# Optimization experiments

Measured on AMD Instinct MI355X. Metric: run time of the kernel, lower is better.

Reference implementation:

```python
import jax, jax.numpy as jnp
import numpy as np

B, Z, A = 1024, 512, 8          # batch_size, z_dim, action_dim
AH, ZH = 64, 512                # action_hidden_dim, z_hidden_dim
N_NEG = 100                     # n_neg_actions
TEMP = 0.1                      # temperature
TOP_K = (1, 3, 10)


def forward_model(z, a, Wa, ba, W1, b1, W2, b2):
    # MLP forward model with skip connection (z_delta=True):
    # embed action, concat with z, 2-layer MLP predicting a delta.
    h_a = jax.nn.relu(a @ Wa + ba)                                   # [..., AH]
    h = jax.nn.relu(jnp.concatenate([jnp.broadcast_to(z, a.shape[:-1] + (Z,)), h_a], axis=-1) @ W1 + b1)  # [..., ZH]
    delta = h @ W2 + b2                                              # [..., Z]
    return z + delta


def setup_inputs() -> dict:
    key = jax.random.key(0)
    ks = jax.random.split(key, 8)
    def w(k, shape, fan_in):
        return jax.random.normal(k, shape, jnp.float32) / np.float32(np.sqrt(fan_in))
    z = jax.random.normal(ks[0], (B, Z), jnp.float32)
    z_next = jax.random.normal(ks[1], (B, Z), jnp.float32)
    z_next_hat = jax.random.normal(ks[2], (B, Z), jnp.float32)
    actions = jax.random.normal(ks[3], (B, A), jnp.float32)
    Wa = w(ks[4], (A, AH), A)
    ba = jnp.zeros((AH,), jnp.float32)
    W1 = w(ks[5], (Z + AH, ZH), Z + AH)
    b1 = jnp.zeros((ZH,), jnp.float32)
    W2 = w(ks[6], (ZH, Z), ZH)
    b2 = jnp.zeros((Z,), jnp.float32)
    return {"z": z, "z_next": z_next, "z_next_hat": z_next_hat, "actions": actions,
            "Wa": Wa, "ba": ba, "W1": W1, "b1": b1, "W2": W2, "b2": b2}


def reference(z, z_next, z_next_hat, actions, Wa, ba, W1, b1, W2, b2):
    # ControlCPC.compute_loss with dot_product_similarity, vectorized:
    # the Python loop over n_neg_actions rolled-action forward-model calls
    # becomes one batched [n-1, B, ...] forward-model evaluation.
    batch = z.shape[0]
    n = min(N_NEG, batch)
    sim = z_next @ z_next_hat.T                                      # [B, B] positives on diagonal
    shifts = jnp.arange(1, n)
    neg_actions = jax.vmap(lambda i: jnp.roll(actions, -i, axis=0))(shifts)  # [n-1, B, A]
    z_hat_neg = forward_model(z[None], neg_actions, Wa, ba, W1, b1, W2, b2)  # [n-1, B, Z]
    neg_sim = jnp.einsum('nbz,bz->bn', z_hat_neg, z_next)            # diag of similarity per shift
    sim_mat = jnp.concatenate([sim, neg_sim], axis=1)                # [B, B+n-1]
    # INCE loss, positives on diagonal
    logp = jax.nn.log_softmax(sim_mat / jnp.float32(TEMP), axis=1)
    loss = -jnp.mean(jnp.diagonal(logp))                             # diagonal takes first B entries
    labels = jnp.arange(batch)[:, None]
    accs = []
    for k in TOP_K:
        _, preds = jax.lax.top_k(sim_mat, k)                         # [B, k]
        accs.append(jnp.mean((preds == labels).astype(jnp.float32)) * k)
    return (loss, accs[0], accs[1], accs[2])
```

## Files before the change

kernel.cpp:

```cpp
#include <hip/hip_runtime.h>
#include <math.h>

#define B_SZ 1024
#define Z_DIM 512
#define A_DIM 8
#define AH 64
#define ZH 512
#define NNEG 99
#define INV_T 10.0f
#define RNP 104

typedef __attribute__((ext_vector_type(8))) short short8;
typedef __attribute__((ext_vector_type(4))) short short4b;
typedef __attribute__((ext_vector_type(4))) float f32x4;

__device__ __forceinline__ short bf16rn(float x) {
    unsigned u = __float_as_uint(x);
    u += 0x7fffu + ((u >> 16) & 1u);
    return (short)(u >> 16);
}
__device__ __forceinline__ void cvt8rn(float4 x0, float4 x1, short8& h) {
    h[0] = bf16rn(x0.x); h[1] = bf16rn(x0.y); h[2] = bf16rn(x0.z); h[3] = bf16rn(x0.w);
    h[4] = bf16rn(x1.x); h[5] = bf16rn(x1.y); h[6] = bf16rn(x1.z); h[7] = bf16rn(x1.w);
}

__device__ __forceinline__ int sw(int m, int kb) { return m * 8 + (kb ^ (m & 7)); }

#define VMWAIT(N) asm volatile("s_waitcnt vmcnt(" #N ")" ::: "memory")
__device__ __forceinline__ void raw_barrier() {
    asm volatile("" ::: "memory");
    __builtin_amdgcn_s_barrier();
    asm volatile("" ::: "memory");
}
typedef const __attribute__((address_space(1))) void* gas_ptr;
typedef __attribute__((address_space(3))) void* las_ptr;
__device__ __forceinline__ void gld_lds16(const void* gsrc, void* ldst) {
    __builtin_amdgcn_global_load_lds((gas_ptr)gsrc, (las_ptr)ldst, 16, 0, 0);
}

__global__ __launch_bounds__(256) void cvt_kernel(
    const float* __restrict__ z, const float* __restrict__ z_next,
    const float* __restrict__ z_next_hat, const float* __restrict__ W1,
    const float* __restrict__ W2, const float* __restrict__ actions,
    const float* __restrict__ Wa, const float* __restrict__ ba,
    short* __restrict__ zb, short* __restrict__ znb, short* __restrict__ znhb,
    short* __restrict__ w1t, short* __restrict__ w2b, short* __restrict__ hab)
{
    const int id = blockIdx.x, tid = threadIdx.x;
    if (id < 896) {
        const float* src; short* dst; int local;
        if (id < 256)      { src = z;          dst = zb;   local = id; }
        else if (id < 512) { src = z_next;     dst = znb;  local = id - 256; }
        else if (id < 768) { src = z_next_hat; dst = znhb; local = id - 512; }
        else               { src = W2;         dst = w2b;  local = id - 768; }
        int i8 = local * 2048 + tid * 8;
        float4 x0 = *(const float4*)&src[i8];
        float4 x1 = *(const float4*)&src[i8 + 4];
        short8 h; cvt8rn(x0, x1, h);
        *(short8*)&dst[i8] = h;
    } else if (id < 968) {
        __shared__ float L[64][68];
        int local = id - 896, kt = local >> 3, nt = local & 7;
#pragma unroll
        for (int i = 0; i < 4; ++i) {
            int f = tid + i * 256;
            int r = f >> 4, c4 = (f & 15) << 2;
            *(float4*)&L[r][c4] = *(const float4*)&W1[(kt * 64 + r) * 512 + nt * 64 + c4];
        }
        __syncthreads();
#pragma unroll
        for (int i = 0; i < 4; ++i) {
            int f = tid + i * 256;
            int r = f >> 4, c4 = (f & 15) << 2;
            short4b o = {bf16rn(L[c4][r]), bf16rn(L[c4 + 1][r]),
                         bf16rn(L[c4 + 2][r]), bf16rn(L[c4 + 3][r])};
            *(short4b*)&w1t[(nt * 64 + r) * 576 + kt * 64 + c4] = o;
        }
    } else {
        __shared__ float sWa[A_DIM * 64];
        __shared__ float sba[64];
        int j0 = (id - 968) * 64;
        for (int i = tid; i < A_DIM * 64; i += 256) sWa[i] = Wa[i];
        if (tid < 64) sba[tid] = ba[tid];
        __syncthreads();
        int r = tid >> 2, c0 = (tid & 3) * 16;
        float4 a0 = *(const float4*)&actions[(j0 + r) * A_DIM + 0];
        float4 a1 = *(const float4*)&actions[(j0 + r) * A_DIM + 4];
        float av[8] = {a0.x, a0.y, a0.z, a0.w, a1.x, a1.y, a1.z, a1.w};
        float o[16];
#pragma unroll
        for (int c = 0; c < 16; ++c) o[c] = sba[c0 + c];
#pragma unroll
        for (int k = 0; k < A_DIM; ++k)
#pragma unroll
            for (int c = 0; c < 16; ++c) o[c] += av[k] * sWa[k * 64 + c0 + c];
#pragma unroll
        for (int c = 0; c < 16; c += 4) {
            short4b h = {bf16rn(fmaxf(o[c], 0.f)),     bf16rn(fmaxf(o[c + 1], 0.f)),
                         bf16rn(fmaxf(o[c + 2], 0.f)), bf16rn(fmaxf(o[c + 3], 0.f))};
            *(short4b*)&hab[(j0 + r) * 64 + c0 + c] = h;
        }
    }
}

__global__ __launch_bounds__(256, 2) void mm_kernel(
    const short* __restrict__ zb, const short* __restrict__ znb,
    const short* __restrict__ znhb, const short* __restrict__ w1t,
    const short* __restrict__ w2b, const short* __restrict__ hab,
    const float* __restrict__ b1,
    float* __restrict__ sim, float* __restrict__ u, float* __restrict__ v,
    float* __restrict__ g)
{
    __shared__ __align__(16) short Ah[128 * 64], Bh[128 * 64];

    const int id = blockIdx.x;
    const int tid = threadIdx.x;

    const short* A; const short* B; const float* bias = nullptr;
    float* C; int N, K, lda, ldb, bm0, bn0;
    if (id < 64) {
        bm0 = (id >> 3) * 128; bn0 = (id & 7) * 128;
        A = znb; lda = 512; B = znhb; ldb = 512; C = sim; N = 1024; K = 512;
    } else if (id < 96) {
        int t = id - 64; bm0 = (t >> 2) * 128; bn0 = (t & 3) * 128;
        A = zb; lda = 512; B = w1t; ldb = 576; C = u; N = 512; K = 512; bias = b1;
    } else if (id < 128) {
        int t = id - 96; bm0 = (t >> 2) * 128; bn0 = (t & 3) * 128;
        A = znb; lda = 512; B = w2b; ldb = 512; C = v; N = 512; K = 512;
    } else {
        int t = id - 128; bm0 = (t >> 2) * 128; bn0 = (t & 3) * 128;
        A = hab; lda = 64; B = w1t + 512; ldb = 576; C = g; N = 512; K = 64;
    }

    const int lane = tid & 63, wv = tid >> 6;
    const int lm = lane & 15, lq = lane >> 4;
    const int wr = (wv >> 1) * 64, wc = (wv & 1) * 64;
    short8* A8 = (short8*)Ah; short8* B8 = (short8*)Bh;
    f32x4 acc[4][4] = {};

    for (int k0 = 0; k0 < K; k0 += 64) {
#pragma unroll
        for (int q = 0; q < 4; ++q) {
            int f = q * 256 + tid;
            int row = f >> 3;
            int ug = (f & 7) ^ (row & 7);
            gld_lds16(&A[(bm0 + row) * lda + k0 + ug * 8],
                      &Ah[(q * 256 + wv * 64) * 8]);
            gld_lds16(&B[(bn0 + row) * ldb + k0 + ug * 8],
                      &Bh[(q * 256 + wv * 64) * 8]);
        }
        VMWAIT(0);
        raw_barrier();
#pragma unroll
        for (int kk = 0; kk < 64; kk += 32) {
            int kbi = (kk >> 3) + lq;
            short8 ah[4], bh[4];
#pragma unroll
            for (int i = 0; i < 4; ++i) ah[i] = A8[sw(wr + i * 16 + lm, kbi)];
#pragma unroll
            for (int j = 0; j < 4; ++j) bh[j] = B8[sw(wc + j * 16 + lm, kbi)];
#pragma unroll
            for (int i = 0; i < 4; ++i)
#pragma unroll
                for (int j = 0; j < 4; ++j)
                    acc[i][j] = __builtin_amdgcn_mfma_f32_16x16x32_bf16(ah[i], bh[j], acc[i][j], 0, 0, 0);
        }
        raw_barrier();
    }
#pragma unroll
    for (int i = 0; i < 4; ++i)
#pragma unroll
        for (int j = 0; j < 4; ++j) {
            int n = bn0 + wc + j * 16 + lm;
            float bb = bias ? bias[n] : 0.0f;
#pragma unroll
            for (int r = 0; r < 4; ++r) {
                int m = bm0 + wr + i * 16 + lq * 4 + r;
                C[m * N + n] = acc[i][j][r] + bb;
            }
        }
}

__global__ __launch_bounds__(64, 4) void neg_kernel(
    const float* __restrict__ u, const float* __restrict__ v,
    const float* __restrict__ g, float* __restrict__ rnall)
{
    const int b = blockIdx.x, t = blockIdx.y;
    const int lane = threadIdx.x;
    const int s0 = 1 + t * 8;

    float4 ga[8], gb[8];
#pragma unroll
    for (int c = 0; c < 8; ++c) {
        int j = (b + s0 + c) & (B_SZ - 1);
        ga[c] = *(const float4*)&g[j * 512 + lane * 4];
        gb[c] = *(const float4*)&g[j * 512 + 256 + lane * 4];
    }
    float4 ua = *(const float4*)&u[b * 512 + lane * 4];
    float4 ub = *(const float4*)&u[b * 512 + 256 + lane * 4];
    float4 va = *(const float4*)&v[b * 512 + lane * 4];
    float4 vb = *(const float4*)&v[b * 512 + 256 + lane * 4];

    float d[8];
#pragma unroll
    for (int c = 0; c < 8; ++c) {
        float s = 0.0f;
        s += fmaxf(ua.x + ga[c].x, 0.0f) * va.x;
        s += fmaxf(ua.y + ga[c].y, 0.0f) * va.y;
        s += fmaxf(ua.z + ga[c].z, 0.0f) * va.z;
        s += fmaxf(ua.w + ga[c].w, 0.0f) * va.w;
        s += fmaxf(ub.x + gb[c].x, 0.0f) * vb.x;
        s += fmaxf(ub.y + gb[c].y, 0.0f) * vb.y;
        s += fmaxf(ub.z + gb[c].z, 0.0f) * vb.z;
        s += fmaxf(ub.w + gb[c].w, 0.0f) * vb.w;
        d[c] = s;
    }
    for (int off = 32; off; off >>= 1) {
#pragma unroll
        for (int c = 0; c < 8; ++c) d[c] += __shfl_down(d[c], off);
    }
    if (lane == 0) {
#pragma unroll
        for (int c = 0; c < 8; ++c)
            if (s0 + c <= NNEG) rnall[b * RNP + s0 + c - 1] = d[c];
    }
}

__global__ __launch_bounds__(256) void smax_kernel(
    const float* __restrict__ sim, const float* __restrict__ rnall,
    const float* __restrict__ z, const float* __restrict__ z_next,
    const float* __restrict__ b2, float* __restrict__ pw)
{
    const int b = blockIdx.x;
    const int tid = threadIdx.x;
    const int w = tid >> 6, lane = tid & 63;
    __shared__ float sred[12];

    float4 s4 = *(const float4*)&sim[b * 1024 + tid * 4];
    float rawn = (tid < NNEG) ? rnall[b * RNP + tid] : 0.0f;
    float diag = sim[b * 1024 + b];

    float2 z2 = *(const float2*)&z[b * 512 + tid * 2];
    float2 n2 = *(const float2*)&z_next[b * 512 + tid * 2];
    float2 c2 = *(const float2*)&b2[tid * 2];
    float p = (z2.x + c2.x) * n2.x + (z2.y + c2.y) * n2.y;
    for (int off = 32; off; off >>= 1) p += __shfl_down(p, off);
    if (lane == 0) sred[w] = p;
    __syncthreads();
    const float c0 = sred[0] + sred[1] + sred[2] + sred[3];
    __syncthreads();

    float neg = (tid < NNEG) ? (rawn + c0) : -3.4e38f;

    float m = fmaxf(fmaxf(s4.x, s4.y), fmaxf(s4.z, s4.w));
    m = fmaxf(m, neg);
    for (int off = 32; off; off >>= 1) m = fmaxf(m, __shfl_xor(m, off));
    if (lane == 0) sred[w] = m;
    __syncthreads();
    m = fmaxf(fmaxf(sred[0], sred[1]), fmaxf(sred[2], sred[3]));

    float es = 0.0f; int ck = 0;
    {
        float xs[4] = {s4.x, s4.y, s4.z, s4.w};
#pragma unroll
        for (int c = 0; c < 4; ++c) {
            int j = tid * 4 + c;
            float x = xs[c];
            es += __expf((x - m) * INV_T);
            if (x > diag) ck++;
            else if (j < b && x == diag) ck++;
        }
    }
    if (tid < NNEG) {
        es += __expf((neg - m) * INV_T);
        if (neg > diag) ck++;
    }
    float ckf = (float)ck;
    for (int off = 32; off; off >>= 1) {
        es += __shfl_down(es, off);
        ckf += __shfl_down(ckf, off);
    }
    if (lane == 0) { sred[4 + w] = es; sred[8 + w] = ckf; }
    __syncthreads();
    if (tid == 0) {
        float est = sred[4] + sred[5] + sred[6] + sred[7];
        int ckt = (int)(sred[8] + sred[9] + sred[10] + sred[11]);
        pw[b * 4 + 0] = (m - diag) * INV_T + logf(est);
        pw[b * 4 + 1] = (ckt < 1) ? 1.0f : 0.0f;
        pw[b * 4 + 2] = (ckt < 3) ? 1.0f : 0.0f;
        pw[b * 4 + 3] = (ckt < 10) ? 1.0f : 0.0f;
    }
}

__global__ __launch_bounds__(256) void final_kernel(
    const float* __restrict__ pw, float* __restrict__ out)
{
    __shared__ float red[256];
    const int tid = threadIdx.x;
    const int c = tid & 3;
    float s = 0.0f;
    for (int r = tid >> 2; r < 1024; r += 64) s += pw[r * 4 + c];
    red[tid] = s;
    __syncthreads();
    if (tid < 4) {
        float t = 0.0f;
        for (int q = 0; q < 64; ++q) t += red[tid + q * 4];
        out[tid] = t * (1.0f / (float)B_SZ);
    }
}

extern "C" void kernel_launch(void* const* d_in, const int* in_sizes, int n_in,
                              void* d_out, int out_size, void* d_ws, size_t ws_size,
                              hipStream_t stream) {
    const float* z          = (const float*)d_in[0];
    const float* z_next     = (const float*)d_in[1];
    const float* z_next_hat = (const float*)d_in[2];
    const float* actions    = (const float*)d_in[3];
    const float* Wa         = (const float*)d_in[4];
    const float* ba         = (const float*)d_in[5];
    const float* W1         = (const float*)d_in[6];
    const float* b1         = (const float*)d_in[7];
    const float* W2         = (const float*)d_in[8];
    const float* b2         = (const float*)d_in[9];
    float* out = (float*)d_out;

    float* ws    = (float*)d_ws;
    float* sim   = ws;
    float* u     = sim + B_SZ * B_SZ;
    float* v     = u + B_SZ * ZH;
    float* g     = v + B_SZ * ZH;
    float* pw    = g + B_SZ * ZH;
    float* rnall = pw + B_SZ * 4;
    short* zb    = (short*)(rnall + B_SZ * RNP);
    short* znb   = zb + B_SZ * Z_DIM;
    short* znhb  = znb + B_SZ * Z_DIM;
    short* w1t   = znhb + B_SZ * Z_DIM;
    short* w2b   = w1t + 512 * 576;
    short* hab   = w2b + 512 * 512;

    cvt_kernel<<<984, 256, 0, stream>>>(z, z_next, z_next_hat, W1, W2,
                                        actions, Wa, ba,
                                        zb, znb, znhb, w1t, w2b, hab);
    mm_kernel<<<160, 256, 0, stream>>>(zb, znb, znhb, w1t, w2b, hab, b1,
                                       sim, u, v, g);
    neg_kernel<<<dim3(B_SZ, 13), 64, 0, stream>>>(u, v, g, rnall);
    smax_kernel<<<B_SZ, 256, 0, stream>>>(sim, rnall, z, z_next, b2, pw);
    final_kernel<<<1, 256, 0, stream>>>(pw, out);
}
```

Before: 114.2 us.

## Tile negative-similarity kernel over batch and shift with shared-memory g rows

Restructures neg_kernel so each 256-thread block covers 16 batch rows and 13 shifts. The overlapping rolled rows of g (28 rows) are staged once in LDS and reused along the diagonal band, and each wave keeps u and v for 4 batch rows in registers. Before, every 64-thread block reloaded 8 g rows from global memory for a single batch row, so this cuts global traffic and block count. In exchange it adds about 57KB of LDS per block, which limits occupancy, plus a serial loop of 13 shifts, each with a cross-lane reduction.

```diff
diff --git a/kernel.cpp b/kernel.cpp
--- a/kernel.cpp
+++ b/kernel.cpp
@@ -9,6 +9,8 @@
 #define NNEG 99
 #define INV_T 10.0f
 #define RNP 104
+#define TBB 16
+#define TSS 13
 
 typedef __attribute__((ext_vector_type(8))) short short8;
 typedef __attribute__((ext_vector_type(4))) short short4b;
@@ -181,48 +183,62 @@
         }
 }
 
-__global__ __launch_bounds__(64, 4) void neg_kernel(
+__global__ __launch_bounds__(256, 2) void neg_kernel(
     const float* __restrict__ u, const float* __restrict__ v,
     const float* __restrict__ g, float* __restrict__ rnall)
 {
-    const int b = blockIdx.x, t = blockIdx.y;
-    const int lane = threadIdx.x;
-    const int s0 = 1 + t * 8;
-
-    float4 ga[8], gb[8];
-#pragma unroll
-    for (int c = 0; c < 8; ++c) {
-        int j = (b + s0 + c) & (B_SZ - 1);
-        ga[c] = *(const float4*)&g[j * 512 + lane * 4];
-        gb[c] = *(const float4*)&g[j * 512 + 256 + lane * 4];
-    }
-    float4 ua = *(const float4*)&u[b * 512 + lane * 4];
-    float4 ub = *(const float4*)&u[b * 512 + 256 + lane * 4];
-    float4 va = *(const float4*)&v[b * 512 + lane * 4];
-    float4 vb = *(const float4*)&v[b * 512 + 256 + lane * 4];
-
-    float d[8];
-#pragma unroll
-    for (int c = 0; c < 8; ++c) {
-        float s = 0.0f;
-        s += fmaxf(ua.x + ga[c].x, 0.0f) * va.x;
-        s += fmaxf(ua.y + ga[c].y, 0.0f) * va.y;
-        s += fmaxf(ua.z + ga[c].z, 0.0f) * va.z;
-        s += fmaxf(ua.w + ga[c].w, 0.0f) * va.w;
-        s += fmaxf(ub.x + gb[c].x, 0.0f) * vb.x;
-        s += fmaxf(ub.y + gb[c].y, 0.0f) * vb.y;
-        s += fmaxf(ub.z + gb[c].z, 0.0f) * vb.z;
-        s += fmaxf(ub.w + gb[c].w, 0.0f) * vb.w;
-        d[c] = s;
-    }
-    for (int off = 32; off; off >>= 1) {
-#pragma unroll
-        for (int c = 0; c < 8; ++c) d[c] += __shfl_down(d[c], off);
-    }
-    if (lane == 0) {
-#pragma unroll
-        for (int c = 0; c < 8; ++c)
-            if (s0 + c <= NNEG) rnall[b * RNP + s0 + c - 1] = d[c];
+    __shared__ float gl[TBB + TSS - 1][512];
+    const int b0 = blockIdx.x * TBB;
+    const int s0 = 1 + blockIdx.y * TSS;
+    const int tid = threadIdx.x;
+    const int w = tid >> 6, lane = tid & 63;
+
+    for (int i = tid; i < (TBB + TSS - 1) * 128; i += 256) {
+        int r = i >> 7, c4 = (i & 127) << 2;
+        int j = (b0 + s0 + r) & (B_SZ - 1);
+        *(float4*)&gl[r][c4] = *(const float4*)&g[j * 512 + c4];
+    }
+
+    const int bb = b0 + w * 4;
+    float4 ua[4], ub[4], va[4], vb[4];
+#pragma unroll
+    for (int i = 0; i < 4; ++i) {
+        ua[i] = *(const float4*)&u[(bb + i) * 512 + lane * 4];
+        ub[i] = *(const float4*)&u[(bb + i) * 512 + 256 + lane * 4];
+        va[i] = *(const float4*)&v[(bb + i) * 512 + lane * 4];
+        vb[i] = *(const float4*)&v[(bb + i) * 512 + 256 + lane * 4];
+    }
+    __syncthreads();
+
+    for (int si = 0; si < TSS; ++si) {
+        int s = s0 + si;
+        if (s > NNEG) break;
+        float d[4];
+#pragma unroll
+        for (int i = 0; i < 4; ++i) {
+            int r = w * 4 + i + si;
+            float4 g0 = *(const float4*)&gl[r][lane * 4];
+            float4 g1 = *(const float4*)&gl[r][256 + lane * 4];
+            float t = 0.0f;
+            t += fmaxf(ua[i].x + g0.x, 0.0f) * va[i].x;
+            t += fmaxf(ua[i].y + g0.y, 0.0f) * va[i].y;
+            t += fmaxf(ua[i].z + g0.z, 0.0f) * va[i].z;
+            t += fmaxf(ua[i].w + g0.w, 0.0f) * va[i].w;
+            t += fmaxf(ub[i].x + g1.x, 0.0f) * vb[i].x;
+            t += fmaxf(ub[i].y + g1.y, 0.0f) * vb[i].y;
+            t += fmaxf(ub[i].z + g1.z, 0.0f) * vb[i].z;
+            t += fmaxf(ub[i].w + g1.w, 0.0f) * vb[i].w;
+            d[i] = t;
+        }
+        for (int off = 32; off; off >>= 1) {
+#pragma unroll
+            for (int i = 0; i < 4; ++i) d[i] += __shfl_down(d[i], off);
+        }
+        if (lane == 0) {
+#pragma unroll
+            for (int i = 0; i < 4; ++i)
+                rnall[(bb + i) * RNP + s - 1] = d[i];
+        }
     }
 }
 
@@ -343,7 +359,7 @@
                                         zb, znb, znhb, w1t, w2b, hab);
     mm_kernel<<<160, 256, 0, stream>>>(zb, znb, znhb, w1t, w2b, hab, b1,
                                        sim, u, v, g);
-    neg_kernel<<<dim3(B_SZ, 13), 64, 0, stream>>>(u, v, g, rnall);
+    neg_kernel<<<dim3(B_SZ / TBB, (NNEG + TSS - 1) / TSS), 256, 0, stream>>>(u, v, g, rnall);
     smax_kernel<<<B_SZ, 256, 0, stream>>>(sim, rnall, z, z_next, b2, pw);
     final_kernel<<<1, 256, 0, stream>>>(pw, out);
 }
```

Measured after the change: 117.6 us. +2.9%, slower.
